# Kernel optimization log

Measured on AMD Instinct MI355X. Metric: run time of the kernel, lower is better.

The kernel has to match this reference:

```python
import jax, jax.numpy as jnp
import numpy as np
import math

N_NODES = 4096
NUM_FEATURES = 500
NHID = 256
RATIO = 0.75


def _build_adj(x):
    # Faithful vectorization of get_threshold/get_edge_index:
    # t = 0.5 * max_{i,j} ||x_i - x_j||^2 ; directed edges (src=i -> dst=j) for j>i with d2<t.
    # Dense adjacency A[dst, src] (jit-friendly; edge count is data-dependent in the original).
    sq = jnp.sum(x * x, axis=1)
    d2 = sq[:, None] + sq[None, :] - 2.0 * (x @ x.T)  # [N,N] squared distances
    t = 0.5 * jnp.max(d2)
    N = x.shape[0]
    lower = jnp.tril(jnp.ones((N, N), dtype=bool), k=-1)  # entry [j,i], j>i
    return jnp.where(lower & (d2 < t), 1.0, 0.0).astype(x.dtype)


def _gcn(A, x, W, b):
    # PyG GCNConv: add self-loops, symmetric normalization D^-1/2 (A+I) D^-1/2, then @ (xW) + b
    N = A.shape[0]
    Ah = A + jnp.eye(N, dtype=A.dtype)
    dis = jax.lax.rsqrt(jnp.sum(Ah, axis=1))  # deg >= 1 due to self loops
    norm = (dis[:, None] * Ah) * dis[None, :]
    return norm @ (x @ W) + b


def _sag_pool(A, x, Wr, Wn, bn, k):
    # SAGPooling with default GraphConv scorer: score = sum-aggr(neighbors)@Wn + bn + x@Wr
    score = jnp.tanh(((A @ x) @ Wn + bn + x @ Wr)[:, 0])  # [N]
    vals, perm = jax.lax.top_k(score, k)  # top ceil(ratio*N) nodes, descending
    xp = x[perm] * vals[:, None]
    Ap = A[perm][:, perm]  # filter edges to surviving nodes
    return Ap, xp


def _readout(x):
    # single graph (batch=None -> all zeros): [gmp, gap] -> [1, 2*nhid]
    return jnp.concatenate([jnp.max(x, axis=0), jnp.mean(x, axis=0)])[None, :]


def setup_inputs() -> dict:
    key = jax.random.key(0)
    ks = jax.random.split(key, 16)
    s = 0.02
    inp = {
        "feature": jax.random.normal(ks[0], (N_NODES, NUM_FEATURES), jnp.float32),
        "img_info": jax.random.normal(ks[1], (N_NODES, 6), jnp.float32),
        "W_pos": jax.random.normal(ks[2], (6, 12), jnp.float32) * s,
        "b_pos": jnp.zeros((12,), jnp.float32),
        "W1": jax.random.normal(ks[3], (512, NHID), jnp.float32) * s,
        "b1": jnp.zeros((NHID,), jnp.float32),
        "W2": jax.random.normal(ks[4], (NHID, NHID), jnp.float32) * s,
        "b2": jnp.zeros((NHID,), jnp.float32),
        "W3": jax.random.normal(ks[5], (NHID, NHID), jnp.float32) * s,
        "b3": jnp.zeros((NHID,), jnp.float32),
        "Wr1": jax.random.normal(ks[6], (NHID, 1), jnp.float32) * s,
        "Wn1": jax.random.normal(ks[7], (NHID, 1), jnp.float32) * s,
        "bs1": jnp.zeros((1,), jnp.float32),
        "Wr2": jax.random.normal(ks[8], (NHID, 1), jnp.float32) * s,
        "Wn2": jax.random.normal(ks[9], (NHID, 1), jnp.float32) * s,
        "bs2": jnp.zeros((1,), jnp.float32),
        "Wr3": jax.random.normal(ks[10], (NHID, 1), jnp.float32) * s,
        "Wn3": jax.random.normal(ks[11], (NHID, 1), jnp.float32) * s,
        "bs3": jnp.zeros((1,), jnp.float32),
    }
    return inp


def reference(feature, img_info, W_pos, b_pos, W1, b1, W2, b2, W3, b3,
              Wr1, Wn1, bs1, Wr2, Wn2, bs2, Wr3, Wn3, bs3):
    pos = jax.nn.relu(img_info @ W_pos + b_pos)          # [N,12]
    feat = jnp.concatenate([feature, pos], axis=1)       # [N,512]
    N = feat.shape[0]
    k1 = math.ceil(RATIO * N)
    k2 = math.ceil(RATIO * k1)
    k3 = math.ceil(RATIO * k2)

    A = _build_adj(feat)

    x = jax.nn.relu(_gcn(A, feat, W1, b1))
    A, x = _sag_pool(A, x, Wr1, Wn1, bs1, k1)
    x1 = _readout(x)

    x = jax.nn.relu(_gcn(A, x, W2, b2))
    A, x = _sag_pool(A, x, Wr2, Wn2, bs2, k2)
    x2 = _readout(x)

    x = jax.nn.relu(_gcn(A, x, W3, b3))
    A, x = _sag_pool(A, x, Wr3, Wn3, bs3, k3)
    x3 = _readout(x)

    return x1 + x2 + x3  # [1, 2*NHID]
```

## Files before the change

kernel.cpp:

```cpp
#include <hip/hip_runtime.h>
#include <hip/hip_bf16.h>
#include <math.h>

typedef __hip_bfloat16 bf16;
typedef unsigned short ushort;
typedef unsigned int uint;
typedef unsigned long long ull;
static __device__ __forceinline__ float b2f(bf16 x){ return __bfloat162float(x); }

static __device__ __forceinline__ float ldf(const void* p, int i, int isbf){
    return isbf ? b2f(((const bf16*)p)[i]) : ((const float*)p)[i];
}
static __device__ __forceinline__ ushort f2b(float x){
    return __bfloat16_as_ushort(__float2bfloat16(x));
}
static __device__ __forceinline__ uint fcode(float v){
    uint u = __float_as_uint(v);
    return (u & 0x80000000u) ? ~u : (u | 0x80000000u);
}
static __device__ __forceinline__ float fdecode(uint c){
    uint u = (c & 0x80000000u) ? (c & 0x7FFFFFFFu) : ~c;
    return __uint_as_float(u);
}

#define NN    4096
#define FEAT0 500
#define DIN   512
#define NH    256
#define KL1   3072
#define KL2   2304
#define KL3   1728
#define EDGE_CAP 786432u

typedef __attribute__((ext_vector_type(8)))  short v8s;
typedef __attribute__((ext_vector_type(16))) float v16f;

static __device__ __forceinline__ void detect_bf16(const void* p, int n, int t,
        uint* flag){
    if (t < 256 && t < n){
        uint e = ((uint)((const ushort*)p)[t] >> 7) & 0xFFu;
        if (e >= 135u) atomicAnd(flag, 0u);
    }
}

struct DtIn { const void* p[19]; int n[19]; };
__global__ __launch_bounds__(512) void k_prep(DtIn da,
        ushort* __restrict__ Xb, float* __restrict__ sq, ushort* __restrict__ Wb,
        unsigned* __restrict__ dflag, float* __restrict__ degA,
        uint* __restrict__ maxU, float* __restrict__ sums,
        unsigned* __restrict__ ecnt, unsigned* __restrict__ maxd2,
        float* __restrict__ tmin){
    int row = blockIdx.x, t = threadIdx.x;
    if (row < NN){
        __shared__ uint fl[4];
        if (t < 4) fl[t] = 1u;
        __syncthreads();
        detect_bf16(da.p[0], da.n[0], t, &fl[0]);
        detect_bf16(da.p[1], da.n[1], t, &fl[1]);
        detect_bf16(da.p[2], da.n[2], t, &fl[2]);
        detect_bf16(da.p[3], da.n[3], t, &fl[3]);
        __syncthreads();
        int f_feat = (int)fl[0], f_img = (int)fl[1], f_wp = (int)fl[2], f_bp = (int)fl[3];
        float v;
        if (t < FEAT0) v = ldf(da.p[0], row*FEAT0 + t, f_feat);
        else {
            int c = t - FEAT0;
            float acc = ldf(da.p[3], c, f_bp);
            #pragma unroll
            for (int d = 0; d < 6; d++)
                acc += ldf(da.p[1], row*6+d, f_img) * ldf(da.p[2], d*12+c, f_wp);
            v = fmaxf(acc, 0.f);
        }
        bf16 vb = __float2bfloat16(v);
        Xb[row*DIN + t] = __bfloat16_as_ushort(vb);
        float vr = b2f(vb);
        __shared__ float red[512];
        red[t] = vr*vr;
        __syncthreads();
        for (int s = 256; s > 0; s >>= 1){ if (t < s) red[t] += red[t+s]; __syncthreads(); }
        if (t == 0) sq[row] = red[0];
    } else if (row < NN + 64){
        __shared__ uint fl[3];
        if (t < 3) fl[t] = 1u;
        __syncthreads();
        detect_bf16(da.p[4], da.n[4], t, &fl[0]);
        detect_bf16(da.p[6], da.n[6], t, &fl[1]);
        detect_bf16(da.p[8], da.n[8], t, &fl[2]);
        __syncthreads();
        int i0 = ((row - NN)*512 + t)*8;
        #pragma unroll
        for (int j = 0; j < 8; j++){
            int idx = i0 + j;
            float v;
            if (idx < 131072)       v = ldf(da.p[4], idx,          (int)fl[0]);
            else if (idx < 196608)  v = ldf(da.p[6], idx - 131072, (int)fl[1]);
            else                    v = ldf(da.p[8], idx - 196608, (int)fl[2]);
            Wb[idx] = __bfloat16_as_ushort(__float2bfloat16(v));
        }
    } else {
        for (int i = t; i < NN; i += 512) degA[i] = 1.0f;
        for (int i = t; i < 4096; i += 512) tmin[i] = INFINITY;
        for (int i = t; i < 768; i += 512){ maxU[i] = 0x007FFFFFu; sums[i] = 0.f; }
        if (t == 0){ ecnt[0]=0u; ecnt[1]=0u; ecnt[2]=0u; ecnt[3]=0u; maxd2[0]=0u; }
        if (t < 19){
            const unsigned short* h = (const unsigned short*)da.p[t];
            int n = da.n[t]; if (n > 256) n = 256;
            int isbf = 1;
            for (int j = 0; j < n; j++){
                uint e = ((uint)h[j] >> 7) & 0xFFu;
                if (e >= 135u) isbf = 0;
            }
            dflag[t] = (unsigned)isbf;
        }
    }
}

static __device__ __forceinline__ v16f mm_tile(const ushort* __restrict__ Arows,
        const ushort* __restrict__ Brows, int K, ushort* As, ushort* Bs,
        int tid, int wv, int l31, int hi){
    int row0 = tid >> 3, g0 = tid & 7;
    int row1 = row0 + 32;
    int d0 = row0*64 + ((g0^(row0&7))<<3);
    int d1 = row1*64 + ((g0^(row1&7))<<3);
    int wwr = wv >> 1, wwc = wv & 1;
    int ra0 = (wwr*32 + l31)*64, rbp = (wwc*32 + l31)*64;
    int fr7a = (wwr*32 + l31) & 7, fr7b = (wwc*32 + l31) & 7;
    float4 a0p = *(const float4*)(Arows + (size_t)row0*K + g0*8);
    float4 a1p = *(const float4*)(Arows + (size_t)row1*K + g0*8);
    float4 b0p = *(const float4*)(Brows + (size_t)row0*K + g0*8);
    float4 b1p = *(const float4*)(Brows + (size_t)row1*K + g0*8);
    v16f acc = {};
    int NC = K >> 6;
    for (int c = 0; c < NC; c++){
        __syncthreads();
        *(float4*)&As[d0] = a0p; *(float4*)&As[d1] = a1p;
        *(float4*)&Bs[d0] = b0p; *(float4*)&Bs[d1] = b1p;
        __syncthreads();
        if (c + 1 < NC){
            int k0 = (c+1)*64;
            a0p = *(const float4*)(Arows + (size_t)row0*K + k0 + g0*8);
            a1p = *(const float4*)(Arows + (size_t)row1*K + k0 + g0*8);
            b0p = *(const float4*)(Brows + (size_t)row0*K + k0 + g0*8);
            b1p = *(const float4*)(Brows + (size_t)row1*K + k0 + g0*8);
        }
        #pragma unroll
        for (int ks = 0; ks < 4; ks++){
            int gq = ks*2 + hi;
            v8s a = *(const v8s*)&As[ra0 + ((gq^fr7a)<<3)];
            v8s b = *(const v8s*)&Bs[rbp + ((gq^fr7b)<<3)];
            acc = __builtin_amdgcn_mfma_f32_32x32x16_bf16(a, b, acc, 0, 0, 0);
        }
    }
    return acc;
}

static __device__ __forceinline__ void xw_body(const ushort* __restrict__ Ab,
        const ushort* __restrict__ Wb, float* __restrict__ XW, int rb, int cb,
        int K, ushort* As, ushort* Bs){
    int tid = threadIdx.x, lane = tid & 63, wv = tid >> 6;
    int wwr = wv >> 1, wwc = wv & 1;
    int l31 = lane & 31, hi = lane >> 5;
    int arow0 = tid >> 3, ag = tid & 7;
    int arow1 = arow0 + 32;
    int da0 = arow0*64 + ((ag^(arow0&7))<<3);
    int da1 = arow1*64 + ((ag^(arow1&7))<<3);
    const size_t baseA = (size_t)rb*64*K;
    int kr = tid >> 2, ng = tid & 3;
    float4 a0p = *(const float4*)(Ab + baseA + (size_t)arow0*K + ag*8);
    float4 a1p = *(const float4*)(Ab + baseA + (size_t)arow1*K + ag*8);
    float4 b0p = *(const float4*)(Wb + (size_t)kr*NH + cb*64 + ng*16);
    float4 b1p = *(const float4*)(Wb + (size_t)kr*NH + cb*64 + ng*16 + 8);
    v16f acc = {};
    int ra0 = (wwr*32 + l31)*64, rbp = (wwc*32 + l31)*64;
    int fr7a = (wwr*32 + l31) & 7, fr7b = (wwc*32 + l31) & 7;
    int kg = kr >> 3, k7 = kr & 7;
    int NC = K >> 6;
    for (int c = 0; c < NC; c++){
        __syncthreads();
        *(float4*)&As[da0] = a0p; *(float4*)&As[da1] = a1p;
        const ushort* bw0 = (const ushort*)&b0p;
        const ushort* bw1 = (const ushort*)&b1p;
        #pragma unroll
        for (int j = 0; j < 8; j++){
            int nn = ng*16 + j;
            Bs[nn*64 + ((kg^(nn&7))<<3) + k7] = bw0[j];
        }
// ... 3 lines not shown
            Bs[nn*64 + ((kg^(nn&7))<<3) + k7] = bw1[j];
        }
        __syncthreads();
        if (c + 1 < NC){
            int k0 = (c+1)*64;
            a0p = *(const float4*)(Ab + baseA + (size_t)arow0*K + k0 + ag*8);
            a1p = *(const float4*)(Ab + baseA + (size_t)arow1*K + k0 + ag*8);
            b0p = *(const float4*)(Wb + (size_t)(k0+kr)*NH + cb*64 + ng*16);
            b1p = *(const float4*)(Wb + (size_t)(k0+kr)*NH + cb*64 + ng*16 + 8);
        }
        #pragma unroll
        for (int ks = 0; ks < 4; ks++){
            int gq = ks*2 + hi;
            v8s a = *(const v8s*)&As[ra0 + ((gq^fr7a)<<3)];
            v8s b = *(const v8s*)&Bs[rbp + ((gq^fr7b)<<3)];
            acc = __builtin_amdgcn_mfma_f32_32x32x16_bf16(a, b, acc, 0, 0, 0);
        }
    }
    int n  = cb*64 + wwc*32 + l31;
    int mb = rb*64 + wwr*32 + 4*hi;
    #pragma unroll
    for (int i = 0; i < 16; i++){
        int m = mb + (i&3) + 8*(i>>2);
        XW[(size_t)m*NH + n] = acc[i];
    }
}

template<int PASS>
__global__ __launch_bounds__(256) void k_gram(const ushort* __restrict__ Xb,
        const float* __restrict__ sq, unsigned* __restrict__ maxd2,
        float* __restrict__ tmin, unsigned* __restrict__ ecnt,
        unsigned* __restrict__ edges, float* __restrict__ deg,
        const ushort* __restrict__ Wb, float* __restrict__ XW){
    __shared__ __align__(16) ushort As[64*64];
    __shared__ __align__(16) ushort Bs[64*64];
    int rb = blockIdx.x, cb = blockIdx.y;
    if (PASS == 1 && cb >= 64){
        xw_body(Xb, Wb, XW, rb, cb - 64, DIN, As, Bs);
        return;
    }
    if (cb > rb) return;
    int tid = threadIdx.x;
    float tthr = 0.f;
    if (PASS == 2){
        tthr = 0.5f * __uint_as_float(maxd2[0]);
        if (tmin[rb*64 + cb] >= tthr) return;
    }
    int lane = tid & 63, wv = tid >> 6;
    int l31 = lane & 31, hi = lane >> 5;
    int wwr = wv >> 1, wwc = wv & 1;
    v16f acc = mm_tile(Xb + (size_t)rb*64*DIN, Xb + (size_t)cb*64*DIN, DIN,
                       As, Bs, tid, wv, l31, hi);
    int rbase = rb*64 + wwr*32 + 4*hi;
    int col   = cb*64 + wwc*32 + l31;
    float sqc = sq[col];
    if (PASS == 1){
        float m = 0.f, mn = INFINITY;
        #pragma unroll
        for (int i = 0; i < 16; i++){
            int r = rbase + (i&3) + 8*(i>>2);
            float d2 = sq[r] + sqc - 2.f*acc[i];
            if (r != col) m = fmaxf(m, d2);
            if (r > col)  mn = fminf(mn, d2);
        }
        #pragma unroll
        for (int off = 32; off >= 1; off >>= 1){
            m  = fmaxf(m,  __shfl_down(m,  off));
            mn = fminf(mn, __shfl_down(mn, off));
        }
        __shared__ float wmax[4], wmin[4];
        if (lane == 0){ wmax[wv] = m; wmin[wv] = mn; }
        __syncthreads();
        if (tid == 0){
            float mm = fmaxf(fmaxf(wmax[0], wmax[1]), fmaxf(wmax[2], wmax[3]));
            tmin[rb*64 + cb] = fminf(fminf(wmin[0], wmin[1]), fminf(wmin[2], wmin[3]));
            atomicMax(maxd2, __float_as_uint(fmaxf(mm, 0.f)));
        }
    } else {
        #pragma unroll
        for (int i = 0; i < 16; i++){
            int r = rbase + (i&3) + 8*(i>>2);
            float d2 = sq[r] + sqc - 2.f*acc[i];
            if (r > col && d2 < tthr){
                unsigned idx = atomicAdd(ecnt, 1u);
                if (idx < EDGE_CAP){
                    edges[idx] = ((unsigned)r << 16) | (unsigned)col;
                    atomicAdd(&deg[r], 1.0f);
                }
            }
        }
    }
}

__global__ __launch_bounds__(256) void k_xwp(const float* __restrict__ Xn,
        const int* __restrict__ perm, const float* __restrict__ svals,
        const ushort* __restrict__ Wb, float* __restrict__ XW, int M,
        uint* __restrict__ maxU, float* __restrict__ sums, int layer){
    int rb = blockIdx.x, cb = blockIdx.y;
    __shared__ __align__(16) ushort As[64*64];
    __shared__ __align__(16) ushort Bs[64*64];
    __shared__ float pmx[256], psm[256];
    int tid = threadIdx.x, lane = tid & 63, wv = tid >> 6;
    int wwr = wv >> 1, wwc = wv & 1;
    int l31 = lane & 31, hi = lane >> 5;
    int arow0 = tid >> 3, ag = tid & 7;
    int arow1 = arow0 + 32;
    int da0 = arow0*64 + ((ag^(arow0&7))<<3);
    int da1 = arow1*64 + ((ag^(arow1&7))<<3);
    int p0 = perm[rb*64 + arow0]; float sv0 = svals[rb*64 + arow0];
    int p1 = perm[rb*64 + arow1]; float sv1 = svals[rb*64 + arow1];
    int kr = tid >> 2, ng = tid & 3;
    int kg = kr >> 3, k7 = kr & 7;
    int ra0 = (wwr*32 + l31)*64, rbp = (wwc*32 + l31)*64;
    int fr7a = (wwr*32 + l31) & 7, fr7b = (wwc*32 + l31) & 7;

    float4 xa0 = *(const float4*)(Xn + (size_t)p0*NH + ag*8);
    float4 xa1 = *(const float4*)(Xn + (size_t)p0*NH + ag*8 + 4);
    float4 xb0 = *(const float4*)(Xn + (size_t)p1*NH + ag*8);
    float4 xb1 = *(const float4*)(Xn + (size_t)p1*NH + ag*8 + 4);
    float4 wb0 = *(const float4*)(Wb + (size_t)kr*NH + cb*64 + ng*16);
// ... 42 lines not shown
            float m = -INFINITY, s = 0.f;
            #pragma unroll
            for (int i = 0; i < 16; i++){
                int rr = q*16 + i;
                float v = __uint_as_float(((uint)As[rr*64 + ((gg^(rr&7))<<3) + c7]) << 16);
                m = fmaxf(m, v); s += v;
            }
            pmx[tid] = m; psm[tid] = s;
            __syncthreads();
            if (tid < 64){
                float mm = fmaxf(fmaxf(pmx[tid], pmx[tid+64]), fmaxf(pmx[tid+128], pmx[tid+192]));
                float ss = psm[tid] + psm[tid+64] + psm[tid+128] + psm[tid+192];
                atomicMax(&maxU[layer*NH + c*64 + tid], fcode(mm));
                atomicAdd(&sums[layer*NH + c*64 + tid], ss);
            }
        }
        #pragma unroll
        for (int ks = 0; ks < 4; ks++){
            int gq = ks*2 + hi;
            v8s a = *(const v8s*)&As[ra0 + ((gq^fr7a)<<3)];
            v8s b = *(const v8s*)&Bs[rbp + ((gq^fr7b)<<3)];
            acc = __builtin_amdgcn_mfma_f32_32x32x16_bf16(a, b, acc, 0, 0, 0);
        }
    }
    int n  = cb*64 + wwc*32 + l31;
    int mb = rb*64 + wwr*32 + 4*hi;
    #pragma unroll
    for (int i = 0; i < 16; i++){
        int m = mb + (i&3) + 8*(i>>2);
        XW[(size_t)m*NH + n] = acc[i];
    }
}

__global__ __launch_bounds__(256) void k_gcnscore(const float* __restrict__ XW,
        const unsigned* __restrict__ edges, const unsigned* __restrict__ ecnt, int slot,
        const float* __restrict__ deg, const void* __restrict__ b,
        const void* __restrict__ Wn, const void* __restrict__ Wr, const void* __restrict__ bs,
        const unsigned* __restrict__ fb, const unsigned* __restrict__ fWn,
        const unsigned* __restrict__ fWr, const unsigned* __restrict__ fbs,
        float* __restrict__ Xn, float* __restrict__ s1, float* __restrict__ z){
    int row = blockIdx.x, t = threadIdx.x;
    __shared__ unsigned eL[256];
    __shared__ unsigned Esh;
    if (t == 0){ unsigned E0 = ecnt[slot]; Esh = (E0 > EDGE_CAP) ? EDGE_CAP : E0; }
    __syncthreads();
    unsigned E = Esh;
    float disr = 1.0f / sqrtf(deg[row]);
    float acc = disr * XW[row*NH + t];
    for (unsigned base = 0; base < E; base += 256){
        unsigned nchunk = E - base; if (nchunk > 256) nchunk = 256;
        __syncthreads();
        if (t < nchunk) eL[t] = edges[base + t];
        __syncthreads();
        for (unsigned j = 0; j < nchunk; j++){
            unsigned ed = eL[j];
            if ((int)(ed >> 16) == row){
                int src = ed & 0xFFFFu;
                acc += (1.0f / sqrtf(deg[src])) * XW[src*NH + t];
            }
        }
    }
    float xn = fmaxf(fmaf(disr, acc, ldf(b, t, (int)fb[0])), 0.f);
    Xn[row*NH + t] = xn;
    float a  = xn * ldf(Wn, t, (int)fWn[0]);
    float bb = xn * ldf(Wr, t, (int)fWr[0]);
    for (int off = 32; off >= 1; off >>= 1){ a += __shfl_down(a, off); bb += __shfl_down(bb, off); }
    __shared__ float ra[4], rbv[4];
    int w = t >> 6;
    if ((t & 63) == 0){ ra[w] = a; rbv[w] = bb; }
    __syncthreads();
    if (t == 0){
        s1[row] = ra[0]+ra[1]+ra[2]+ra[3];
        z[row]  = rbv[0]+rbv[1]+rbv[2]+rbv[3] + ldf(bs, 0, (int)fbs[0]);
    }
}

static __device__ __forceinline__ uint2 radix_scan(const uint* hist, uint* wt,
        uint* ws, uint* sh, int t, int lane, int wv, uint kk, int NB){
    uint loc = 0;
    int b0 = t << 2;
    if (b0 < NB) loc = hist[b0] + hist[b0+1] + hist[b0+2] + hist[b0+3];
    uint s = loc;
    #pragma unroll
    for (int off = 1; off < 64; off <<= 1){
        uint u = __shfl_down(s, off);
        if (lane + off < 64) s += u;
    }
    if (lane == 0) wt[wv] = s;
    __syncthreads();
    if (t < 16){
        uint a = 0;
        for (int j = t + 1; j < 16; j++) a += wt[j];
        ws[t] = a;
    }
    __syncthreads();
    if (b0 < NB){
        uint run = ws[wv] + (s - loc);
        for (int b = b0 + 3; b >= b0; b--){
            uint h = hist[b];
            if (run < kk && run + h >= kk){ sh[0] = (uint)b; sh[1] = run; }
            run += h;
        }
    }
    __syncthreads();
    return make_uint2(sh[0], sh[1]);
}

__global__ __launch_bounds__(1024) void k_select(const float* __restrict__ z,
        const float* __restrict__ s1, int N, int k,
        const unsigned* __restrict__ eIn, unsigned* __restrict__ ecnt, int slotCur,
        unsigned* __restrict__ eOut, int slotOut,
        int* __restrict__ perm, float* __restrict__ svals,
        float* __restrict__ degN, int Nnext){
    __shared__ float zsh[4096];
    __shared__ int   rnk[4096];
    __shared__ uint  hist[4096];
    __shared__ uint  wcnt[16];
    __shared__ uint  wbase[16];
    __shared__ uint  sh[4];
    int t = threadIdx.x;
    int lane = t & 63, wv = t >> 6;
    for (int i = t; i < N; i += 1024){ zsh[i] = z[i]; rnk[i] = -1; }
    for (int i = t; i < Nnext; i += 1024) degN[i] = 1.0f;
    if (t == 0) sh[2] = 0u;
    __syncthreads();
    unsigned E = ecnt[slotCur]; if (E > EDGE_CAP) E = EDGE_CAP;
    for (unsigned e = t; e < E; e += 1024){
        unsigned ed = eIn[e];
        atomicAdd(&zsh[ed >> 16], s1[ed & 0xFFFFu]);
    }
    __syncthreads();
    bool v0 = t < N,        v1 = t+1024 < N,  v2 = t+2048 < N,  v3 = t+3072 < N;
    uint c0 = v0 ? fcode(zsh[t])      : 0u;
    uint c1 = v1 ? fcode(zsh[t+1024]) : 0u;
    uint c2 = v2 ? fcode(zsh[t+2048]) : 0u;
    uint c3 = v3 ? fcode(zsh[t+3072]) : 0u;

    for (int i = t; i < 4096; i += 1024) hist[i] = 0u;
    __syncthreads();
    if (v0) atomicAdd(&hist[c0 >> 20], 1u);
    if (v1) atomicAdd(&hist[c1 >> 20], 1u);
    if (v2) atomicAdd(&hist[c2 >> 20], 1u);
    if (v3) atomicAdd(&hist[c3 >> 20], 1u);
    __syncthreads();
    uint2 p1 = radix_scan(hist, wcnt, wbase, sh, t, lane, wv, (uint)k, 4096);
    uint B1 = p1.x; uint kk2 = (uint)k - p1.y;
    for (int i = t; i < 4096; i += 1024) hist[i] = 0u;
    __syncthreads();
    if (v0 && (c0 >> 20) == B1) atomicAdd(&hist[(c0 >> 8) & 0xFFFu], 1u);
    if (v1 && (c1 >> 20) == B1) atomicAdd(&hist[(c1 >> 8) & 0xFFFu], 1u);
    if (v2 && (c2 >> 20) == B1) atomicAdd(&hist[(c2 >> 8) & 0xFFFu], 1u);
    if (v3 && (c3 >> 20) == B1) atomicAdd(&hist[(c3 >> 8) & 0xFFFu], 1u);
    __syncthreads();
    uint2 p2 = radix_scan(hist, wcnt, wbase, sh, t, lane, wv, kk2, 4096);
    uint B2 = p2.x; uint kk3 = kk2 - p2.y;
    uint hi24 = (B1 << 12) | B2;
    for (int i = t; i < 256; i += 1024) hist[i] = 0u;
    __syncthreads();
    if (v0 && (c0 >> 8) == hi24) atomicAdd(&hist[c0 & 0xFFu], 1u);
    if (v1 && (c1 >> 8) == hi24) atomicAdd(&hist[c1 & 0xFFu], 1u);
    if (v2 && (c2 >> 8) == hi24) atomicAdd(&hist[c2 & 0xFFu], 1u);
    if (v3 && (c3 >> 8) == hi24) atomicAdd(&hist[c3 & 0xFFu], 1u);
    __syncthreads();
    uint2 p3 = radix_scan(hist, wcnt, wbase, sh, t, lane, wv, kk3, 256);
    uint T = (B1 << 20) | (B2 << 8) | p3.x;

    ull b0 = __ballot(v0 && c0 > T), b1 = __ballot(v1 && c1 > T);
    ull b2 = __ballot(v2 && c2 > T), b3 = __ballot(v3 && c3 > T);
    uint t0 = (uint)__popcll(b0), t1 = (uint)__popcll(b1);
    uint t2 = (uint)__popcll(b2), t3 = (uint)__popcll(b3);
    if (lane == 0) wcnt[wv] = t0 + t1 + t2 + t3;
    __syncthreads();
    if (t == 0){
        uint s = 0;
        for (int i = 0; i < 16; i++){ wbase[i] = s; s += wcnt[i]; }
        sh[1] = s;
    }
    __syncthreads();
    uint cntGT = sh[1];
    uint rem = (uint)k - cntGT;
    ull ltm = ((ull)1 << lane) - 1;
    uint off = wbase[wv];
    if (v0 && c0 > T){ uint r = off + (uint)__popcll(b0 & ltm); int i = t;
        perm[r] = i; svals[r] = tanhf(zsh[i]); rnk[i] = (int)r; }
    off += t0;
    if (v1 && c1 > T){ uint r = off + (uint)__popcll(b1 & ltm); int i = t+1024;
        perm[r] = i; svals[r] = tanhf(zsh[i]); rnk[i] = (int)r; }
    off += t1;
    if (v2 && c2 > T){ uint r = off + (uint)__popcll(b2 & ltm); int i = t+2048;
        perm[r] = i; svals[r] = tanhf(zsh[i]); rnk[i] = (int)r; }
    off += t2;
    if (v3 && c3 > T){ uint r = off + (uint)__popcll(b3 & ltm); int i = t+3072;
        perm[r] = i; svals[r] = tanhf(zsh[i]); rnk[i] = (int)r; }
    #pragma unroll
    for (int j = 0; j < 4; j++){
        int i = t + j*1024;
        bool vv = (j==0) ? v0 : (j==1) ? v1 : (j==2) ? v2 : v3;
        uint cc = (j==0) ? c0 : (j==1) ? c1 : (j==2) ? c2 : c3;
        if (vv && cc == T){
            uint e = atomicAdd(&sh[2], 1u);
            if (e < rem){
                uint r = cntGT + e;
                perm[r] = i; svals[r] = tanhf(zsh[i]); rnk[i] = (int)r;
            }
        }
    }
    __syncthreads();
    if (slotOut >= 0){
        for (unsigned e = t; e < E; e += 1024){
            unsigned ed = eIn[e];
            int nd = rnk[ed >> 16], ns = rnk[ed & 0xFFFFu];
            if (nd >= 0 && ns >= 0){
                unsigned idx = atomicAdd(&ecnt[slotOut], 1u);
                if (idx < EDGE_CAP){
                    eOut[idx] = ((unsigned)nd << 16) | (unsigned)ns;
                    atomicAdd(&degN[nd], 1.0f);
                }
            }
        }
    }
}

__global__ __launch_bounds__(256) void k_poolread3(const float* __restrict__ Xn,
        const int* __restrict__ perm, const float* __restrict__ svals, int k,
        uint* __restrict__ maxU, float* __restrict__ sums,
        unsigned* __restrict__ done, float* __restrict__ out){
    int b = blockIdx.x, t = threadIdx.x;
    float m = -INFINITY, s = 0.f;
    for (int r = b; r < k; r += 64){
        int p = perm[r];
        float v = Xn[p*NH + t] * svals[r];
        m = fmaxf(m, v); s += v;
    }
    atomicMax(&maxU[2*NH + t], fcode(m));
    atomicAdd(&sums[2*NH + t], s);
    __threadfence();
    __shared__ uint lastv;
    if (t == 0) lastv = atomicAdd(done, 1u);
    __syncthreads();
    if (lastv == 63u){
        uint m0 = atomicAdd(&maxU[t], 0u);
        uint m1 = atomicAdd(&maxU[NH + t], 0u);
        uint m2 = atomicAdd(&maxU[2*NH + t], 0u);
// ... 2 lines not shown
        float s2 = atomicAdd(&sums[2*NH + t], 0.f);
        out[t] = fdecode(m0) + fdecode(m1) + fdecode(m2);
        out[NH + t] = s0*(1.0f/KL1) + s1v*(1.0f/KL2) + s2*(1.0f/KL3);
    }
}

extern "C" void kernel_launch(void* const* d_in, const int* in_sizes, int n_in,
                              void* d_out, int out_size, void* d_ws, size_t ws_size,
                              hipStream_t stream)
{
    const void* b1 = d_in[5];
    const void* b2 = d_in[7];
    const void* b3 = d_in[9];
    const void* Wr1 = d_in[10]; const void* Wn1 = d_in[11]; const void* bs1 = d_in[12];
    const void* Wr2 = d_in[13]; const void* Wn2 = d_in[14]; const void* bs2 = d_in[15];
    const void* Wr3 = d_in[16]; const void* Wn3 = d_in[17]; const void* bs3 = d_in[18];

    char* w = (char*)d_ws;
    auto alloc = [&](size_t bytes)->char*{ char* p = w; w += (bytes + 255) & ~(size_t)255; return p; };
    ushort*   Xb    = (ushort*)  alloc((size_t)NN*DIN*2);
    float*    Xn    = (float*)   alloc((size_t)NN*NH*4);
    float*    XW    = (float*)   alloc((size_t)NN*NH*4);
    ushort*   Wb    = (ushort*)  alloc((size_t)262144*2);
    unsigned* E0    = (unsigned*)alloc((size_t)EDGE_CAP*4);
    unsigned* E1    = (unsigned*)alloc((size_t)EDGE_CAP*4);
    float*    tmin  = (float*)   alloc(4096*4);
    float*    sq    = (float*)   alloc(NN*4);
    float*    degA  = (float*)   alloc(NN*4);
    float*    degB  = (float*)   alloc(NN*4);
    float*    s1    = (float*)   alloc(NN*4);
    float*    z     = (float*)   alloc(NN*4);
    int*      perm  = (int*)     alloc(NN*4);
    float*    svals = (float*)   alloc(NN*4);
    unsigned* ecnt  = (unsigned*)alloc(256);
    unsigned* maxd2 = (unsigned*)alloc(256);
    unsigned* dflag = (unsigned*)alloc(256);
    uint*     maxU  = (uint*)    alloc(768*4);
    float*    sums  = (float*)   alloc(768*4);
    (void)ws_size;

    DtIn da;
    for (int i = 0; i < 19; i++){ da.p[i] = d_in[i]; da.n[i] = in_sizes[i]; }

    k_prep<<<NN + 65, 512, 0, stream>>>(da, Xb, sq, Wb, dflag, degA, maxU, sums,
            ecnt, maxd2, tmin);
    k_gram<1><<<dim3(64,68), 256, 0, stream>>>(Xb, sq, maxd2, tmin, ecnt, E0, degA,
            Wb, XW);
    k_gram<2><<<dim3(64,64), 256, 0, stream>>>(Xb, sq, maxd2, tmin, ecnt, E0, degA,
            Wb, XW);

    k_gcnscore<<<NN, 256, 0, stream>>>(XW, E0, ecnt, 0, degA, b1, Wn1, Wr1, bs1,
            dflag+5, dflag+11, dflag+10, dflag+12, Xn, s1, z);
    k_select<<<1, 1024, 0, stream>>>(z, s1, NN, KL1, E0, ecnt, 0, E1, 1,
            perm, svals, degB, KL1);

    k_xwp<<<dim3(48,4), 256, 0, stream>>>(Xn, perm, svals, Wb + 131072, XW, KL1,
            maxU, sums, 0);
    k_gcnscore<<<KL1, 256, 0, stream>>>(XW, E1, ecnt, 1, degB, b2, Wn2, Wr2, bs2,
            dflag+7, dflag+14, dflag+13, dflag+15, Xn, s1, z);
    k_select<<<1, 1024, 0, stream>>>(z, s1, KL1, KL2, E1, ecnt, 1, E0, 2,
            perm, svals, degA, KL2);

    k_xwp<<<dim3(36,4), 256, 0, stream>>>(Xn, perm, svals, Wb + 196608, XW, KL2,
            maxU, sums, 1);
    k_gcnscore<<<KL2, 256, 0, stream>>>(XW, E0, ecnt, 2, degA, b3, Wn3, Wr3, bs3,
            dflag+9, dflag+17, dflag+16, dflag+18, Xn, s1, z);
    k_select<<<1, 1024, 0, stream>>>(z, s1, KL2, KL3, E0, ecnt, 2,
            (unsigned*)nullptr, -1, perm, svals, degB, 0);
    k_poolread3<<<64, 256, 0, stream>>>(Xn, perm, svals, KL3, maxU, sums,
            ecnt + 3, (float*)d_out);
}
```

Before: 236.8 us.

## Fuse top-k selection into GCN scoring via last-block pattern; triangular gram grid

Merges the single-block k_select kernel into k_gcnscore: every block increments a done counter, and the last block to finish does the edge aggregation, radix top-k and edge filtering with 256 threads, using a global rnk array instead of shared memory. The gram kernels now launch a 1D triangular grid (2080 tiles) instead of a 64x64 grid where upper-triangle blocks exited early. The row-norm reduction in prep switches to wave shuffles. This removes three kernel launches and the empty blocks, but the serial selection now runs on 256 threads instead of 1024 and reads z/s1 through global atomics, so the tail block may take longer.

```diff
diff --git a/kernel.cpp b/kernel.cpp
--- a/kernel.cpp
+++ b/kernel.cpp
@@ -31,6 +31,7 @@
 #define KL2   2304
 #define KL3   1728
 #define EDGE_CAP 786432u
+#define NTRI  2080
 
 typedef __attribute__((ext_vector_type(8)))  short v8s;
 typedef __attribute__((ext_vector_type(16))) float v16f;
@@ -74,11 +75,18 @@
         bf16 vb = __float2bfloat16(v);
         Xb[row*DIN + t] = __bfloat16_as_ushort(vb);
         float vr = b2f(vb);
-        __shared__ float red[512];
-        red[t] = vr*vr;
-        __syncthreads();
-        for (int s = 256; s > 0; s >>= 1){ if (t < s) red[t] += red[t+s]; __syncthreads(); }
-        if (t == 0) sq[row] = red[0];
+        float vsq = vr*vr;
+        #pragma unroll
+        for (int off = 32; off >= 1; off >>= 1) vsq += __shfl_down(vsq, off);
+        __shared__ float red[8];
+        if ((t & 63) == 0) red[t >> 6] = vsq;
+        __syncthreads();
+        if (t == 0){
+            float sres = 0.f;
+            #pragma unroll
+            for (int i = 0; i < 8; i++) sres += red[i];
+            sq[row] = sres;
+        }
     } else if (row < NN + 64){
         __shared__ uint fl[3];
         if (t < 3) fl[t] = 1u;
@@ -101,7 +109,11 @@
         for (int i = t; i < NN; i += 512) degA[i] = 1.0f;
         for (int i = t; i < 4096; i += 512) tmin[i] = INFINITY;
         for (int i = t; i < 768; i += 512){ maxU[i] = 0x007FFFFFu; sums[i] = 0.f; }
-        if (t == 0){ ecnt[0]=0u; ecnt[1]=0u; ecnt[2]=0u; ecnt[3]=0u; maxd2[0]=0u; }
+        if (t == 0){
+            #pragma unroll
+            for (int i = 0; i < 8; i++) ecnt[i] = 0u;
+            maxd2[0] = 0u;
+        }
         if (t < 19){
             const unsigned short* h = (const unsigned short*)da.p[t];
             int n = da.n[t]; if (n > 256) n = 256;
@@ -223,12 +235,20 @@
         const ushort* __restrict__ Wb, float* __restrict__ XW){
     __shared__ __align__(16) ushort As[64*64];
     __shared__ __align__(16) ushort Bs[64*64];
-    int rb = blockIdx.x, cb = blockIdx.y;
-    if (PASS == 1 && cb >= 64){
-        xw_body(Xb, Wb, XW, rb, cb - 64, DIN, As, Bs);
-        return;
-    }
-    if (cb > rb) return;
+    int b = blockIdx.x;
+    if (PASS == 1){
+        if (b < 256){
+            xw_body(Xb, Wb, XW, b >> 2, b & 3, DIN, As, Bs);
+            return;
+        }
+        b -= 256;
+    }
+    float ff = sqrtf(8.f*(float)b + 1.f);
+    int rb = (int)((ff - 1.f) * 0.5f);
+    while ((rb+1)*(rb+2)/2 <= b) rb++;
+    while (rb*(rb+1)/2 > b) rb--;
+    int cb = b - rb*(rb+1)/2;
+
     int tid = threadIdx.x;
     float tthr = 0.f;
     if (PASS == 2){
@@ -383,16 +403,52 @@
     }
 }
 
-__global__ __launch_bounds__(256) void k_gcnscore(const float* __restrict__ XW,
-        const unsigned* __restrict__ edges, const unsigned* __restrict__ ecnt, int slot,
+static __device__ __forceinline__ uint2 rscan256(const uint* hist, uint* wcnt,
+        uint* sh, int t, int lane, int wv, uint kk, int G){
+    int b0 = t * G;
+    uint loc = 0;
+    for (int j = 0; j < G; j++) loc += hist[b0 + j];
+    uint s = loc;
+    #pragma unroll
+    for (int off = 1; off < 64; off <<= 1){
+        uint u = __shfl_down(s, off);
+        if (lane + off < 64) s += u;
+    }
+    if (lane == 0) wcnt[wv] = s;
+    __syncthreads();
+    uint aw = 0;
+    for (int w = wv + 1; w < 4; w++) aw += wcnt[w];
+    uint run = aw + (s - loc);
+    for (int bb = b0 + G - 1; bb >= b0; bb--){
+        uint h = hist[bb];
+        if (run < kk && run + h >= kk){ sh[0] = (uint)bb; sh[1] = run; }
+        run += h;
+    }
+    __syncthreads();
+    uint2 r; r.x = sh[0]; r.y = sh[1];
+    __syncthreads();
+    return r;
+}
+
+__global__ __launch_bounds__(256) void k_gcnsel(const float* __restrict__ XW,
+        const unsigned* __restrict__ edges, unsigned* __restrict__ ecnt, int slot,
         const float* __restrict__ deg, const void* __restrict__ b,
         const void* __restrict__ Wn, const void* __restrict__ Wr, const void* __restrict__ bs,
         const unsigned* __restrict__ fb, const unsigned* __restrict__ fWn,
         const unsigned* __restrict__ fWr, const unsigned* __restrict__ fbs,
-        float* __restrict__ Xn, float* __restrict__ s1, float* __restrict__ z){
+        float* __restrict__ Xn, float* __restrict__ s1, float* __restrict__ z,
+        int N, int k, unsigned* __restrict__ eOut, int slotOut,
+        int* __restrict__ perm, float* __restrict__ svals,
+        float* __restrict__ degN, int Nnext, int* __restrict__ rnk,
+        unsigned* __restrict__ doneCtr){
     int row = blockIdx.x, t = threadIdx.x;
+    int lane = t & 63, wv = t >> 6;
     __shared__ unsigned eL[256];
     __shared__ unsigned Esh;
+    __shared__ float ra[4], rbv[4];
+    __shared__ uint hist[4096];
+    __shared__ uint wcnt[4], sh[4];
+    __shared__ uint isLast;
     if (t == 0){ unsigned E0 = ecnt[slot]; Esh = (E0 > EDGE_CAP) ? EDGE_CAP : E0; }
     __syncthreads();
     unsigned E = Esh;
@@ -416,150 +472,103 @@
     float a  = xn * ldf(Wn, t, (int)fWn[0]);
     float bb = xn * ldf(Wr, t, (int)fWr[0]);
     for (int off = 32; off >= 1; off >>= 1){ a += __shfl_down(a, off); bb += __shfl_down(bb, off); }
-    __shared__ float ra[4], rbv[4];
-    int w = t >> 6;
-    if ((t & 63) == 0){ ra[w] = a; rbv[w] = bb; }
+    if ((t & 63) == 0){ ra[wv] = a; rbv[wv] = bb; }
     __syncthreads();
     if (t == 0){
         s1[row] = ra[0]+ra[1]+ra[2]+ra[3];
         z[row]  = rbv[0]+rbv[1]+rbv[2]+rbv[3] + ldf(bs, 0, (int)fbs[0]);
     }
-}
-
-static __device__ __forceinline__ uint2 radix_scan(const uint* hist, uint* wt,
-        uint* ws, uint* sh, int t, int lane, int wv, uint kk, int NB){
-    uint loc = 0;
-    int b0 = t << 2;
-    if (b0 < NB) loc = hist[b0] + hist[b0+1] + hist[b0+2] + hist[b0+3];
-    uint s = loc;
-    #pragma unroll
-    for (int off = 1; off < 64; off <<= 1){
-        uint u = __shfl_down(s, off);
-        if (lane + off < 64) s += u;
-    }
-    if (lane == 0) wt[wv] = s;
-    __syncthreads();
-    if (t < 16){
-        uint a = 0;
-        for (int j = t + 1; j < 16; j++) a += wt[j];
-        ws[t] = a;
-    }
-    __syncthreads();
-    if (b0 < NB){
-        uint run = ws[wv] + (s - loc);
-        for (int b = b0 + 3; b >= b0; b--){
-            uint h = hist[b];
-            if (run < kk && run + h >= kk){ sh[0] = (uint)b; sh[1] = run; }
-            run += h;
-        }
-    }
-    __syncthreads();
-    return make_uint2(sh[0], sh[1]);
-}
-
-__global__ __launch_bounds__(1024) void k_select(const float* __restrict__ z,
-        const float* __restrict__ s1, int N, int k,
-        const unsigned* __restrict__ eIn, unsigned* __restrict__ ecnt, int slotCur,
-        unsigned* __restrict__ eOut, int slotOut,
-        int* __restrict__ perm, float* __restrict__ svals,
-        float* __restrict__ degN, int Nnext){
-    __shared__ float zsh[4096];
-    __shared__ int   rnk[4096];
-    __shared__ uint  hist[4096];
-    __shared__ uint  wcnt[16];
-    __shared__ uint  wbase[16];
-    __shared__ uint  sh[4];
-    int t = threadIdx.x;
-    int lane = t & 63, wv = t >> 6;
-    for (int i = t; i < N; i += 1024){ zsh[i] = z[i]; rnk[i] = -1; }
-    for (int i = t; i < Nnext; i += 1024) degN[i] = 1.0f;
+    __syncthreads();
+    if (t == 0){
+        __threadfence();
+        uint old = atomicAdd(doneCtr, 1u);
+        isLast = (old == (uint)(gridDim.x - 1)) ? 1u : 0u;
+    }
+    __syncthreads();
+    if (!isLast) return;
+    __threadfence();
+
+    for (int i = t; i < N; i += 256) rnk[i] = -1;
+    for (int i = t; i < Nnext; i += 256) degN[i] = 1.0f;
     if (t == 0) sh[2] = 0u;
-    __syncthreads();
-    unsigned E = ecnt[slotCur]; if (E > EDGE_CAP) E = EDGE_CAP;
-    for (unsigned e = t; e < E; e += 1024){
-        unsigned ed = eIn[e];
-        atomicAdd(&zsh[ed >> 16], s1[ed & 0xFFFFu]);
-    }
-    __syncthreads();
-    bool v0 = t < N,        v1 = t+1024 < N,  v2 = t+2048 < N,  v3 = t+3072 < N;
-    uint c0 = v0 ? fcode(zsh[t])      : 0u;
-    uint c1 = v1 ? fcode(zsh[t+1024]) : 0u;
-    uint c2 = v2 ? fcode(zsh[t+2048]) : 0u;
-    uint c3 = v3 ? fcode(zsh[t+3072]) : 0u;
-
-    for (int i = t; i < 4096; i += 1024) hist[i] = 0u;
-    __syncthreads();
-    if (v0) atomicAdd(&hist[c0 >> 20], 1u);
-    if (v1) atomicAdd(&hist[c1 >> 20], 1u);
-    if (v2) atomicAdd(&hist[c2 >> 20], 1u);
-    if (v3) atomicAdd(&hist[c3 >> 20], 1u);
-    __syncthreads();
-    uint2 p1 = radix_scan(hist, wcnt, wbase, sh, t, lane, wv, (uint)k, 4096);
+    for (unsigned e = t; e < E; e += 256){
+        unsigned ed = edges[e];
+        float sv = atomicAdd(&s1[ed & 0xFFFFu], 0.f);
+        float old = atomicAdd(&z[ed >> 16], sv);
+        asm volatile("" :: "v"(old));
+    }
+    __syncthreads();
+    uint c[16];
+    #pragma unroll
+    for (int j = 0; j < 16; j++){
+        int i = t + j*256;
+        c[j] = (i < N) ? fcode(atomicAdd(&z[i], 0.f)) : 0u;
+    }
+    for (int i = t; i < 4096; i += 256) hist[i] = 0u;
+    __syncthreads();
+    #pragma unroll
+    for (int j = 0; j < 16; j++)
+        if (t + j*256 < N) atomicAdd(&hist[c[j] >> 20], 1u);
+    __syncthreads();
+    uint2 p1 = rscan256(hist, wcnt, sh, t, lane, wv, (uint)k, 16);
     uint B1 = p1.x; uint kk2 = (uint)k - p1.y;
-    for (int i = t; i < 4096; i += 1024) hist[i] = 0u;
-    __syncthreads();
-    if (v0 && (c0 >> 20) == B1) atomicAdd(&hist[(c0 >> 8) & 0xFFFu], 1u);
-    if (v1 && (c1 >> 20) == B1) atomicAdd(&hist[(c1 >> 8) & 0xFFFu], 1u);
-    if (v2 && (c2 >> 20) == B1) atomicAdd(&hist[(c2 >> 8) & 0xFFFu], 1u);
-    if (v3 && (c3 >> 20) == B1) atomicAdd(&hist[(c3 >> 8) & 0xFFFu], 1u);
-    __syncthreads();
-    uint2 p2 = radix_scan(hist, wcnt, wbase, sh, t, lane, wv, kk2, 4096);
+    for (int i = t; i < 4096; i += 256) hist[i] = 0u;
+    __syncthreads();
+    #pragma unroll
+    for (int j = 0; j < 16; j++)
+        if (t + j*256 < N && (c[j] >> 20) == B1) atomicAdd(&hist[(c[j] >> 8) & 0xFFFu], 1u);
+    __syncthreads();
+    uint2 p2 = rscan256(hist, wcnt, sh, t, lane, wv, kk2, 16);
     uint B2 = p2.x; uint kk3 = kk2 - p2.y;
     uint hi24 = (B1 << 12) | B2;
-    for (int i = t; i < 256; i += 1024) hist[i] = 0u;
-    __syncthreads();
-    if (v0 && (c0 >> 8) == hi24) atomicAdd(&hist[c0 & 0xFFu], 1u);
-    if (v1 && (c1 >> 8) == hi24) atomicAdd(&hist[c1 & 0xFFu], 1u);
-    if (v2 && (c2 >> 8) == hi24) atomicAdd(&hist[c2 & 0xFFu], 1u);
-    if (v3 && (c3 >> 8) == hi24) atomicAdd(&hist[c3 & 0xFFu], 1u);
-    __syncthreads();
-    uint2 p3 = radix_scan(hist, wcnt, wbase, sh, t, lane, wv, kk3, 256);
+    for (int i = t; i < 256; i += 256) hist[i] = 0u;
+    __syncthreads();
+    #pragma unroll
+    for (int j = 0; j < 16; j++)
+        if (t + j*256 < N && (c[j] >> 8) == hi24) atomicAdd(&hist[c[j] & 0xFFu], 1u);
+    __syncthreads();
+    uint2 p3 = rscan256(hist, wcnt, sh, t, lane, wv, kk3, 1);
     uint T = (B1 << 20) | (B2 << 8) | p3.x;
 
-    ull b0 = __ballot(v0 && c0 > T), b1 = __ballot(v1 && c1 > T);
-    ull b2 = __ballot(v2 && c2 > T), b3 = __ballot(v3 && c3 > T);
-    uint t0 = (uint)__popcll(b0), t1 = (uint)__popcll(b1);
-    uint t2 = (uint)__popcll(b2), t3 = (uint)__popcll(b3);
-    if (lane == 0) wcnt[wv] = t0 + t1 + t2 + t3;
-    __syncthreads();
-    if (t == 0){
-        uint s = 0;
-        for (int i = 0; i < 16; i++){ wbase[i] = s; s += wcnt[i]; }
-        sh[1] = s;
-    }
-    __syncthreads();
-    uint cntGT = sh[1];
-    uint rem = (uint)k - cntGT;
-    ull ltm = ((ull)1 << lane) - 1;
-    uint off = wbase[wv];
-    if (v0 && c0 > T){ uint r = off + (uint)__popcll(b0 & ltm); int i = t;
-        perm[r] = i; svals[r] = tanhf(zsh[i]); rnk[i] = (int)r; }
-    off += t0;
-    if (v1 && c1 > T){ uint r = off + (uint)__popcll(b1 & ltm); int i = t+1024;
-        perm[r] = i; svals[r] = tanhf(zsh[i]); rnk[i] = (int)r; }
-    off += t1;
-    if (v2 && c2 > T){ uint r = off + (uint)__popcll(b2 & ltm); int i = t+2048;
-        perm[r] = i; svals[r] = tanhf(zsh[i]); rnk[i] = (int)r; }
-    off += t2;
-    if (v3 && c3 > T){ uint r = off + (uint)__popcll(b3 & ltm); int i = t+3072;
-        perm[r] = i; svals[r] = tanhf(zsh[i]); rnk[i] = (int)r; }
-    #pragma unroll
-    for (int j = 0; j < 4; j++){
-        int i = t + j*1024;
-        bool vv = (j==0) ? v0 : (j==1) ? v1 : (j==2) ? v2 : v3;
-        uint cc = (j==0) ? c0 : (j==1) ? c1 : (j==2) ? c2 : c3;
-        if (vv && cc == T){
+    uint cnt = 0;
+    #pragma unroll
+    for (int j = 0; j < 16; j++)
+        if (t + j*256 < N && c[j] > T) cnt++;
+    uint inc = cnt;
+    #pragma unroll
+    for (int off = 1; off < 64; off <<= 1){
+        uint u = __shfl_up(inc, off);
+        if (lane >= off) inc += u;
+    }
+    if (lane == 63) wcnt[wv] = inc;
+    __syncthreads();
+    uint wb = 0;
+    for (int w = 0; w < wv; w++) wb += wcnt[w];
+    uint total = wcnt[0] + wcnt[1] + wcnt[2] + wcnt[3];
+    uint r = wb + inc - cnt;
+    #pragma unroll
+    for (int j = 0; j < 16; j++){
+        int i = t + j*256;
+        if (i < N && c[j] > T){
+            perm[r] = i; svals[r] = tanhf(fdecode(c[j])); rnk[i] = (int)r; r++;
+        }
+    }
+    uint cntGT = total, rem = (uint)k - cntGT;
+    #pragma unroll
+    for (int j = 0; j < 16; j++){
+        int i = t + j*256;
+        if (i < N && c[j] == T){
             uint e = atomicAdd(&sh[2], 1u);
             if (e < rem){
-                uint r = cntGT + e;
-                perm[r] = i; svals[r] = tanhf(zsh[i]); rnk[i] = (int)r;
+                uint rr = cntGT + e;
+                perm[rr] = i; svals[rr] = tanhf(fdecode(c[j])); rnk[i] = (int)rr;
             }
         }
     }
     __syncthreads();
     if (slotOut >= 0){
-        for (unsigned e = t; e < E; e += 1024){
-            unsigned ed = eIn[e];
+        for (unsigned e = t; e < E; e += 256){
+            unsigned ed = edges[e];
             int nd = rnk[ed >> 16], ns = rnk[ed & 0xFFFFu];
             if (nd >= 0 && ns >= 0){
                 unsigned idx = atomicAdd(&ecnt[slotOut], 1u);
@@ -628,6 +637,7 @@
     float*    z     = (float*)   alloc(NN*4);
     int*      perm  = (int*)     alloc(NN*4);
     float*    svals = (float*)   alloc(NN*4);
+    int*      rnk   = (int*)     alloc(NN*4);
     unsigned* ecnt  = (unsigned*)alloc(256);
     unsigned* maxd2 = (unsigned*)alloc(256);
     unsigned* dflag = (unsigned*)alloc(256);
@@ -640,29 +650,26 @@
 
     k_prep<<<NN + 65, 512, 0, stream>>>(da, Xb, sq, Wb, dflag, degA, maxU, sums,
             ecnt, maxd2, tmin);
-    k_gram<1><<<dim3(64,68), 256, 0, stream>>>(Xb, sq, maxd2, tmin, ecnt, E0, degA,
+    k_gram<1><<<256 + NTRI, 256, 0, stream>>>(Xb, sq, maxd2, tmin, ecnt, E0, degA,
             Wb, XW);
-    k_gram<2><<<dim3(64,64), 256, 0, stream>>>(Xb, sq, maxd2, tmin, ecnt, E0, degA,
+    k_gram<2><<<NTRI, 256, 0, stream>>>(Xb, sq, maxd2, tmin, ecnt, E0, degA,
             Wb, XW);
 
-    k_gcnscore<<<NN, 256, 0, stream>>>(XW, E0, ecnt, 0, degA, b1, Wn1, Wr1, bs1,
-            dflag+5, dflag+11, dflag+10, dflag+12, Xn, s1, z);
-    k_select<<<1, 1024, 0, stream>>>(z, s1, NN, KL1, E0, ecnt, 0, E1, 1,
-            perm, svals, degB, KL1);
+    k_gcnsel<<<NN, 256, 0, stream>>>(XW, E0, ecnt, 0, degA, b1, Wn1, Wr1, bs1,
+            dflag+5, dflag+11, dflag+10, dflag+12, Xn, s1, z,
+            NN, KL1, E1, 1, perm, svals, degB, KL1, rnk, ecnt+4);
 
     k_xwp<<<dim3(48,4), 256, 0, stream>>>(Xn, perm, svals, Wb + 131072, XW, KL1,
             maxU, sums, 0);
-    k_gcnscore<<<KL1, 256, 0, stream>>>(XW, E1, ecnt, 1, degB, b2, Wn2, Wr2, bs2,
-            dflag+7, dflag+14, dflag+13, dflag+15, Xn, s1, z);
-    k_select<<<1, 1024, 0, stream>>>(z, s1, KL1, KL2, E1, ecnt, 1, E0, 2,
-            perm, svals, degA, KL2);
+    k_gcnsel<<<KL1, 256, 0, stream>>>(XW, E1, ecnt, 1, degB, b2, Wn2, Wr2, bs2,
+            dflag+7, dflag+14, dflag+13, dflag+15, Xn, s1, z,
+            KL1, KL2, E0, 2, perm, svals, degA, KL2, rnk, ecnt+5);
 
     k_xwp<<<dim3(36,4), 256, 0, stream>>>(Xn, perm, svals, Wb + 196608, XW, KL2,
             maxU, sums, 1);
-    k_gcnscore<<<KL2, 256, 0, stream>>>(XW, E0, ecnt, 2, degA, b3, Wn3, Wr3, bs3,
-            dflag+9, dflag+17, dflag+16, dflag+18, Xn, s1, z);
-    k_select<<<1, 1024, 0, stream>>>(z, s1, KL2, KL3, E0, ecnt, 2,
-            (unsigned*)nullptr, -1, perm, svals, degB, 0);
+    k_gcnsel<<<KL2, 256, 0, stream>>>(XW, E0, ecnt, 2, degA, b3, Wn3, Wr3, bs3,
+            dflag+9, dflag+17, dflag+16, dflag+18, Xn, s1, z,
+            KL2, KL3, (unsigned*)nullptr, -1, perm, svals, degB, 0, rnk, ecnt+6);
     k_poolread3<<<64, 256, 0, stream>>>(Xn, perm, svals, KL3, maxU, sums,
             ecnt + 3, (float*)d_out);
 }
```

Measured after the change: 420.5 us. 77.6% more time.

## Use 128x128 gram tiles over a compact lower-triangle grid

Applied to the files above, without the earlier changes.

The distance gram kernel now computes 128x128 tiles, with each wave doing a 2x2 grid of MFMA 32x32 subtiles. Blocks are launched only over the lower-triangular tile pairs, using a triangular index decode, instead of launching a full 64x64 grid and exiting early above the diagonal. Each loaded fragment is reused across more MFMAs and far fewer blocks are launched. The trade-off is more registers and LDS per block, and coarser early-exit skipping in the second pass. The squared-norm reduction in prep also switches from a shared-memory tree to wave shuffles.

```diff
diff --git a/kernel.cpp b/kernel.cpp
--- a/kernel.cpp
+++ b/kernel.cpp
@@ -31,6 +31,7 @@
 #define KL2   2304
 #define KL3   1728
 #define EDGE_CAP 786432u
+#define NT32  528
 
 typedef __attribute__((ext_vector_type(8)))  short v8s;
 typedef __attribute__((ext_vector_type(16))) float v16f;
@@ -74,11 +75,18 @@
         bf16 vb = __float2bfloat16(v);
         Xb[row*DIN + t] = __bfloat16_as_ushort(vb);
         float vr = b2f(vb);
-        __shared__ float red[512];
-        red[t] = vr*vr;
-        __syncthreads();
-        for (int s = 256; s > 0; s >>= 1){ if (t < s) red[t] += red[t+s]; __syncthreads(); }
-        if (t == 0) sq[row] = red[0];
+        float vsq = vr*vr;
+        #pragma unroll
+        for (int off = 32; off >= 1; off >>= 1) vsq += __shfl_down(vsq, off);
+        __shared__ float red[8];
+        if ((t & 63) == 0) red[t >> 6] = vsq;
+        __syncthreads();
+        if (t == 0){
+            float sres = 0.f;
+            #pragma unroll
+            for (int i = 0; i < 8; i++) sres += red[i];
+            sq[row] = sres;
+        }
     } else if (row < NN + 64){
         __shared__ uint fl[3];
         if (t < 3) fl[t] = 1u;
@@ -101,7 +109,11 @@
         for (int i = t; i < NN; i += 512) degA[i] = 1.0f;
         for (int i = t; i < 4096; i += 512) tmin[i] = INFINITY;
         for (int i = t; i < 768; i += 512){ maxU[i] = 0x007FFFFFu; sums[i] = 0.f; }
-        if (t == 0){ ecnt[0]=0u; ecnt[1]=0u; ecnt[2]=0u; ecnt[3]=0u; maxd2[0]=0u; }
+        if (t == 0){
+            #pragma unroll
+            for (int i = 0; i < 8; i++) ecnt[i] = 0u;
+            maxd2[0] = 0u;
+        }
         if (t < 19){
             const unsigned short* h = (const unsigned short*)da.p[t];
             int n = da.n[t]; if (n > 256) n = 256;
@@ -113,45 +125,6 @@
             dflag[t] = (unsigned)isbf;
         }
     }
-}
-
-static __device__ __forceinline__ v16f mm_tile(const ushort* __restrict__ Arows,
-        const ushort* __restrict__ Brows, int K, ushort* As, ushort* Bs,
-        int tid, int wv, int l31, int hi){
-    int row0 = tid >> 3, g0 = tid & 7;
-    int row1 = row0 + 32;
-    int d0 = row0*64 + ((g0^(row0&7))<<3);
-    int d1 = row1*64 + ((g0^(row1&7))<<3);
-    int wwr = wv >> 1, wwc = wv & 1;
-    int ra0 = (wwr*32 + l31)*64, rbp = (wwc*32 + l31)*64;
-    int fr7a = (wwr*32 + l31) & 7, fr7b = (wwc*32 + l31) & 7;
-    float4 a0p = *(const float4*)(Arows + (size_t)row0*K + g0*8);
-    float4 a1p = *(const float4*)(Arows + (size_t)row1*K + g0*8);
-    float4 b0p = *(const float4*)(Brows + (size_t)row0*K + g0*8);
-    float4 b1p = *(const float4*)(Brows + (size_t)row1*K + g0*8);
-    v16f acc = {};
-    int NC = K >> 6;
-    for (int c = 0; c < NC; c++){
-        __syncthreads();
-        *(float4*)&As[d0] = a0p; *(float4*)&As[d1] = a1p;
-        *(float4*)&Bs[d0] = b0p; *(float4*)&Bs[d1] = b1p;
-        __syncthreads();
-        if (c + 1 < NC){
-            int k0 = (c+1)*64;
-            a0p = *(const float4*)(Arows + (size_t)row0*K + k0 + g0*8);
-            a1p = *(const float4*)(Arows + (size_t)row1*K + k0 + g0*8);
-            b0p = *(const float4*)(Brows + (size_t)row0*K + k0 + g0*8);
-            b1p = *(const float4*)(Brows + (size_t)row1*K + k0 + g0*8);
-        }
-        #pragma unroll
-        for (int ks = 0; ks < 4; ks++){
-            int gq = ks*2 + hi;
-            v8s a = *(const v8s*)&As[ra0 + ((gq^fr7a)<<3)];
-            v8s b = *(const v8s*)&Bs[rbp + ((gq^fr7b)<<3)];
-            acc = __builtin_amdgcn_mfma_f32_32x32x16_bf16(a, b, acc, 0, 0, 0);
-        }
-    }
-    return acc;
 }
 
 static __device__ __forceinline__ void xw_body(const ushort* __restrict__ Ab,
@@ -221,36 +194,94 @@
         float* __restrict__ tmin, unsigned* __restrict__ ecnt,
         unsigned* __restrict__ edges, float* __restrict__ deg,
         const ushort* __restrict__ Wb, float* __restrict__ XW){
-    __shared__ __align__(16) ushort As[64*64];
-    __shared__ __align__(16) ushort Bs[64*64];
-    int rb = blockIdx.x, cb = blockIdx.y;
-    if (PASS == 1 && cb >= 64){
-        xw_body(Xb, Wb, XW, rb, cb - 64, DIN, As, Bs);
-        return;
-    }
-    if (cb > rb) return;
+    __shared__ __align__(16) ushort As[2*4096];
+    __shared__ __align__(16) ushort Bs[2*4096];
+    int b = blockIdx.x;
+    if (PASS == 1){
+        if (b < 256){
+            xw_body(Xb, Wb, XW, b >> 2, b & 3, DIN, As, Bs);
+            return;
+        }
+        b -= 256;
+    }
+    float ff = sqrtf(8.f*(float)b + 1.f);
+    int rb = (int)((ff - 1.f) * 0.5f);
+    while ((rb+1)*(rb+2)/2 <= b) rb++;
+    while (rb*(rb+1)/2 > b) rb--;
+    int cb = b - rb*(rb+1)/2;
+
     int tid = threadIdx.x;
     float tthr = 0.f;
     if (PASS == 2){
         tthr = 0.5f * __uint_as_float(maxd2[0]);
-        if (tmin[rb*64 + cb] >= tthr) return;
+        if (tmin[rb*32 + cb] >= tthr) return;
     }
     int lane = tid & 63, wv = tid >> 6;
     int l31 = lane & 31, hi = lane >> 5;
-    int wwr = wv >> 1, wwc = wv & 1;
-    v16f acc = mm_tile(Xb + (size_t)rb*64*DIN, Xb + (size_t)cb*64*DIN, DIN,
-                       As, Bs, tid, wv, l31, hi);
-    int rbase = rb*64 + wwr*32 + 4*hi;
-    int col   = cb*64 + wwc*32 + l31;
-    float sqc = sq[col];
+    int qr = wv >> 1, qc = wv & 1;
+    int r0 = tid >> 3, g0 = tid & 7;
+    const ushort* Ar = Xb + (size_t)rb*128*DIN;
+    const ushort* Br = Xb + (size_t)cb*128*DIN;
+    float4 ap[4], bp[4];
+    #pragma unroll
+    for (int j = 0; j < 4; j++){
+        ap[j] = *(const float4*)(Ar + (size_t)(r0+32*j)*DIN + g0*8);
+        bp[j] = *(const float4*)(Br + (size_t)(r0+32*j)*DIN + g0*8);
+    }
+    v16f acc[2][2] = {};
+    for (int c = 0; c < DIN/64; c++){
+        __syncthreads();
+        #pragma unroll
+        for (int j = 0; j < 4; j++){
+            int row = r0 + 32*j;
+            int st = row >> 6, lr = row & 63;
+            int dst = st*4096 + lr*64 + ((g0^(lr&7))<<3);
+            *(float4*)&As[dst] = ap[j];
+            *(float4*)&Bs[dst] = bp[j];
+        }
+        __syncthreads();
+        if (c + 1 < DIN/64){
+            int k0 = (c+1)*64;
+            #pragma unroll
+            for (int j = 0; j < 4; j++){
+                ap[j] = *(const float4*)(Ar + (size_t)(r0+32*j)*DIN + k0 + g0*8);
+                bp[j] = *(const float4*)(Br + (size_t)(r0+32*j)*DIN + k0 + g0*8);
+            }
+        }
+        #pragma unroll
+        for (int ks = 0; ks < 4; ks++){
+            int gq = ks*2 + hi;
+            #pragma unroll
+            for (int sr = 0; sr < 2; sr++){
+                int ar_ = sr*32 + l31;
+                v8s av = *(const v8s*)&As[qr*4096 + ar_*64 + ((gq^(ar_&7))<<3)];
+                #pragma unroll
+                for (int sc = 0; sc < 2; sc++){
+                    int br_ = sc*32 + l31;
+                    v8s bv = *(const v8s*)&Bs[qc*4096 + br_*64 + ((gq^(br_&7))<<3)];
+                    acc[sr][sc] = __builtin_amdgcn_mfma_f32_32x32x16_bf16(av, bv, acc[sr][sc], 0, 0, 0);
+                }
+            }
+        }
+    }
+    int rb128 = rb*128, cb128 = cb*128;
     if (PASS == 1){
         float m = 0.f, mn = INFINITY;
         #pragma unroll
-        for (int i = 0; i < 16; i++){
-            int r = rbase + (i&3) + 8*(i>>2);
-            float d2 = sq[r] + sqc - 2.f*acc[i];
-            if (r != col) m = fmaxf(m, d2);
-            if (r > col)  mn = fminf(mn, d2);
+        for (int sr = 0; sr < 2; sr++){
+            int rbase = rb128 + qr*64 + sr*32 + 4*hi;
+            #pragma unroll
+            for (int sc = 0; sc < 2; sc++){
+                int col = cb128 + qc*64 + sc*32 + l31;
+                float sqc = sq[col];
+                #pragma unroll
+                for (int i = 0; i < 16; i++){
+                    int r = rbase + (i&3) + 8*(i>>2);
+                    float d2 = sq[r] + sqc - 2.f*acc[sr][sc][i];
+                    if (r != col) m = fmaxf(m, d2);
+                    if (r > col)  mn = fminf(mn, d2);
+                }
+            }
         }
         #pragma unroll
         for (int off = 32; off >= 1; off >>= 1){
@@ -262,19 +293,28 @@
         __syncthreads();
         if (tid == 0){
             float mm = fmaxf(fmaxf(wmax[0], wmax[1]), fmaxf(wmax[2], wmax[3]));
-            tmin[rb*64 + cb] = fminf(fminf(wmin[0], wmin[1]), fminf(wmin[2], wmin[3]));
+            tmin[rb*32 + cb] = fminf(fminf(wmin[0], wmin[1]), fminf(wmin[2], wmin[3]));
             atomicMax(maxd2, __float_as_uint(fmaxf(mm, 0.f)));
         }
     } else {
         #pragma unroll
-        for (int i = 0; i < 16; i++){
-            int r = rbase + (i&3) + 8*(i>>2);
-            float d2 = sq[r] + sqc - 2.f*acc[i];
-            if (r > col && d2 < tthr){
-                unsigned idx = atomicAdd(ecnt, 1u);
-                if (idx < EDGE_CAP){
-                    edges[idx] = ((unsigned)r << 16) | (unsigned)col;
-                    atomicAdd(&deg[r], 1.0f);
+        for (int sr = 0; sr < 2; sr++){
+            int rbase = rb128 + qr*64 + sr*32 + 4*hi;
+            #pragma unroll
+            for (int sc = 0; sc < 2; sc++){
+                int col = cb128 + qc*64 + sc*32 + l31;
+                float sqc = sq[col];
+                #pragma unroll
+                for (int i = 0; i < 16; i++){
+                    int r = rbase + (i&3) + 8*(i>>2);
+                    float d2 = sq[r] + sqc - 2.f*acc[sr][sc][i];
+                    if (r > col && d2 < tthr){
+                        unsigned idx = atomicAdd(ecnt, 1u);
+                        if (idx < EDGE_CAP){
+                            edges[idx] = ((unsigned)r << 16) | (unsigned)col;
+                            atomicAdd(&deg[r], 1.0f);
+                        }
+                    }
                 }
             }
         }
@@ -640,9 +680,9 @@
 
     k_prep<<<NN + 65, 512, 0, stream>>>(da, Xb, sq, Wb, dflag, degA, maxU, sums,
             ecnt, maxd2, tmin);
-    k_gram<1><<<dim3(64,68), 256, 0, stream>>>(Xb, sq, maxd2, tmin, ecnt, E0, degA,
+    k_gram<1><<<256 + NT32, 256, 0, stream>>>(Xb, sq, maxd2, tmin, ecnt, E0, degA,
             Wb, XW);
-    k_gram<2><<<dim3(64,64), 256, 0, stream>>>(Xb, sq, maxd2, tmin, ecnt, E0, degA,
+    k_gram<2><<<NT32, 256, 0, stream>>>(Xb, sq, maxd2, tmin, ecnt, E0, degA,
             Wb, XW);
 
     k_gcnscore<<<NN, 256, 0, stream>>>(XW, E0, ecnt, 0, degA, b1, Wn1, Wr1, bs1,
```

Result: slower. 276.9 us (+16.9%).
